# Kernel tuning notes

Measured on AMD Instinct MI355X. Metric: run time of the kernel, lower is better.

The kernel has to match this reference:

```python
import jax, jax.numpy as jnp
import numpy as np

B, S, D, MD = 4, 4096, 1024, 512
SCALE = 0.02  # init scale for weights


def _layernorm(x, g, b, eps=1e-5):
    m = jnp.mean(x, axis=-1, keepdims=True)
    v = jnp.mean((x - m) ** 2, axis=-1, keepdims=True)
    return (x - m) * jax.lax.rsqrt(v + eps) * g + b


def _mem_mlp(h, W0, W1):
    # MemoryMLP depth=2: linear -> gelu -> linear (no biases)
    return jax.nn.gelu(h @ W0) @ W1


def _assoc_scan(gates, inputs):
    # state_t = g_t * state_{t-1} + in_t, over the seq axis (axis=1)
    def step(state, gi):
        g, i = gi
        s = g * state + i
        return s, s
    init = jnp.zeros_like(inputs[:, 0])
    _, out = jax.lax.scan(step, init, (jnp.moveaxis(gates, 1, 0), jnp.moveaxis(inputs, 1, 0)))
    return jnp.moveaxis(out, 1, 0)


def setup_inputs() -> dict:
    key = jax.random.key(0)
    ks = jax.random.split(key, 10)
    return {
        "x": jax.random.normal(ks[0], (B, S, D), jnp.float32),
        "Wd": jax.random.normal(ks[1], (D, MD), jnp.float32) * SCALE,
        "bd": jnp.zeros((MD,), jnp.float32),
        "Wu": jax.random.normal(ks[2], (MD, D), jnp.float32) * SCALE,
        "bu": jnp.zeros((D,), jnp.float32),
        "Wq": jax.random.normal(ks[3], (MD, MD), jnp.float32) * SCALE,
        "bq": jnp.zeros((MD,), jnp.float32),
        "Wk": jax.random.normal(ks[4], (MD, MD), jnp.float32) * SCALE,
        "bk": jnp.zeros((MD,), jnp.float32),
        "Wv": jax.random.normal(ks[5], (MD, MD), jnp.float32) * SCALE,
        "bv": jnp.zeros((MD,), jnp.float32),
        "q_gamma": jnp.ones((MD,), jnp.float32),
        "q_beta": jnp.zeros((MD,), jnp.float32),
        "k_gamma": jnp.ones((MD,), jnp.float32),
        "k_beta": jnp.zeros((MD,), jnp.float32),
        "W0": jax.random.normal(ks[6], (MD, MD), jnp.float32) * SCALE,
        "W1": jax.random.normal(ks[7], (MD, MD), jnp.float32) * SCALE,
        "adaptive_lr": jnp.full((1,), 0.01, jnp.float32),
        "forget_factor": jnp.full((1,), 0.1, jnp.float32),
    }


def reference(x, Wd, bd, Wu, bu, Wq, bq, Wk, bk, Wv, bv,
              q_gamma, q_beta, k_gamma, k_beta, W0, W1,
              adaptive_lr, forget_factor):
    h = x @ Wd + bd                                   # [B,S,MD] down_proj
    q = _layernorm(h @ Wq + bq, q_gamma, q_beta)      # q_norm(to_queries)
    k = _layernorm(h @ Wk + bk, k_gamma, k_beta)      # k_norm(to_keys)
    v = h @ Wv + bv                                   # to_values
    retrieved = _mem_mlp(q, W0, W1)                   # memory read
    pred = _mem_mlp(k, W0, W1)                        # memory store pred
    # per-token surprise: MSE over feature dim
    surprise = jnp.mean((pred - v) ** 2, axis=-1, keepdims=True)  # [B,S,1]
    gate_val = 1.0 - jax.nn.sigmoid(forget_factor)[0]
    gates = jnp.full((B, S, 1), 1.0, jnp.float32) * gate_val
    inputs = adaptive_lr[0] * surprise * v            # surprise-weighted write
    scanned = _assoc_scan(gates, inputs)              # sequential recurrence
    out = (retrieved + scanned) @ Wu + bu             # up_proj
    return out
```

## Files before the change

### kernel.cpp

```cpp
#include <hip/hip_runtime.h>
#include <hip/hip_bf16.h>
#include <math.h>

#define B_    4
#define S_    4096
#define DD    1024
#define MD    512
#define NTOK  16384
#define CHUNK 32
#define NCH   128

typedef unsigned short u16;
typedef unsigned int u32;
typedef __attribute__((ext_vector_type(8))) short short8;
typedef __attribute__((ext_vector_type(4))) float f32x4;
typedef __attribute__((ext_vector_type(4))) unsigned short us4;

__device__ __forceinline__ float bf2f(u16 u) {
    u32 x = ((u32)u) << 16;
    return __builtin_bit_cast(float, x);
}
__device__ __forceinline__ u16 f2bf(float f) {
    u32 x = __builtin_bit_cast(u32, f);
    u32 lsb = (x >> 16) & 1u;
    x += 0x7fffu + lsb;
    return (u16)(x >> 16);
}
__device__ __forceinline__ float gelu_f(float x) {
    float x3 = x * x * x;
    return 0.5f * x * (1.0f + tanhf(0.7978845608028654f * (x + 0.044715f * x3)));
}
__device__ __forceinline__ float gate_from_ff(const float* ff) {
    return 1.0f - 1.0f / (1.0f + expf(-ff[0]));
}

#define GLDS(gp, lp) __builtin_amdgcn_global_load_lds( \
    (const __attribute__((address_space(1))) void*)(gp), \
    (__attribute__((address_space(3))) void*)(lp), 16, 0, 0)

template<int EPI, int HB, int OUTBF>
__global__ __launch_bounds__(256) void gemm_bf16_k(
    const u16* __restrict__ A0, const u16* __restrict__ A1, const u16* __restrict__ A2,
    const u16* __restrict__ W0p, const u16* __restrict__ W1p, const u16* __restrict__ W2p,
    const float* __restrict__ c0, const float* __restrict__ c1, const float* __restrict__ c2,
    void* __restrict__ o0, void* __restrict__ o1, void* __restrict__ o2,
    int K, int gx, int OM)
{
    __shared__ __align__(16) u16 Al[3][128 * 32];
    __shared__ __align__(16) u16 Bl[3][128 * 32];
    const int tid = threadIdx.x;
    const int w = tid >> 6, l = tid & 63;

    const int z = blockIdx.z;
    const u16* A      = (z == 0) ? A0 : (z == 1) ? A1 : A2;
    const u16* BT     = (z == 0) ? W0p : (z == 1) ? W1p : W2p;
    const float* bias = (z == 0) ? c0 : (z == 1) ? c1 : c2;
    void* outp        = (z == 0) ? o0 : (z == 1) ? o1 : o2;

    const int nwg = gridDim.x;
    const int cpx = nwg >> 3;
    const int o = blockIdx.x;
    const int swz = (o & 7) * cpx + (o >> 3);
    const int bx = swz % gx, by = swz / gx;

    const int rowBase = by * 128, colBase = bx * 128;
    const int wm = (w >> 1) * 64, wn = (w & 1) * 64;
    const int lr = l & 15;

    float bj[4] = {0.f, 0.f, 0.f, 0.f};
    if (HB) {
#pragma unroll
        for (int n = 0; n < 4; ++n) bj[n] = bias[colBase + wn + n * 16 + lr];
        asm volatile("" :: "v"(bj[0]), "v"(bj[1]), "v"(bj[2]), "v"(bj[3]));
    }
    asm volatile("s_waitcnt vmcnt(0)" ::: "memory");
    __builtin_amdgcn_sched_barrier(0);

    const int srow = l >> 2;
    const int skoff = ((l & 3) ^ (srow & 3)) * 8;
    const u16* Ag0 = A  + (size_t)(rowBase + w * 16 + srow) * K + skoff;
    const u16* Ag1 = A  + (size_t)(rowBase + (w + 4) * 16 + srow) * K + skoff;
    const u16* Bg0 = BT + (size_t)(colBase + w * 16 + srow) * K + skoff;
    const u16* Bg1 = BT + (size_t)(colBase + (w + 4) * 16 + srow) * K + skoff;

    f32x4 acc[4][4];
#pragma unroll
    for (int i = 0; i < 4; ++i)
#pragma unroll
        for (int j = 0; j < 4; ++j) acc[i][j] = (f32x4){0.f, 0.f, 0.f, 0.f};

    const int KT = K >> 5;

#define STAGE(kt, buf) do { \
    const size_t ko = (size_t)(kt) << 5; \
    GLDS(Ag0 + ko, &Al[buf][(w * 16) * 32]); \
    GLDS(Ag1 + ko, &Al[buf][((w + 4) * 16) * 32]); \
    GLDS(Bg0 + ko, &Bl[buf][(w * 16) * 32]); \
    GLDS(Bg1 + ko, &Bl[buf][((w + 4) * 16) * 32]); \
} while (0)

    STAGE(0, 0);
    STAGE(1, 1);
    asm volatile("s_waitcnt vmcnt(4)" ::: "memory");
    __builtin_amdgcn_sched_barrier(0);
    __builtin_amdgcn_s_barrier();
    __builtin_amdgcn_sched_barrier(0);

    const int rsw = (((l >> 4) ^ (l & 3)) << 3);
    int bt = 0;
    for (int t = 0; t < KT; ++t) {
        int bs = bt + 2; if (bs >= 3) bs -= 3;
        const bool more = (t + 2) < KT;
        if (more) STAGE(t + 2, bs);
        short8 af[4], bfr[4];
#pragma unroll
        for (int m = 0; m < 4; ++m)
            af[m] = *(const short8*)&Al[bt][(wm + m * 16 + lr) * 32 + rsw];
#pragma unroll
        for (int n = 0; n < 4; ++n)
            bfr[n] = *(const short8*)&Bl[bt][(wn + n * 16 + lr) * 32 + rsw];
#pragma unroll
        for (int m = 0; m < 4; ++m)
#pragma unroll
            for (int n = 0; n < 4; ++n)
                acc[m][n] = __builtin_amdgcn_mfma_f32_16x16x32_bf16(af[m], bfr[n], acc[m][n], 0, 0, 0);
        if (more) { asm volatile("s_waitcnt vmcnt(4)" ::: "memory"); }
        else      { asm volatile("s_waitcnt vmcnt(0)" ::: "memory"); }
        __builtin_amdgcn_sched_barrier(0);
        __builtin_amdgcn_s_barrier();
        __builtin_amdgcn_sched_barrier(0);
        bt = (bt + 1 == 3) ? 0 : bt + 1;
    }
#undef STAGE

    const int g4 = (l >> 4) * 4;
    const int col0 = colBase + wn;

    if (OUTBF) {
        u16* scr = &Al[0][0] + w * 1024;
        u16* ob = (u16*)outp;
        const bool odd = l & 1;
        const int lrp = lr & ~1;
#pragma unroll
        for (int m = 0; m < 4; ++m) {
            const int baseRow = rowBase + wm + m * 16;
            float vq[4][4];
#pragma unroll
            for (int n = 0; n < 4; ++n) {
#pragma unroll
                for (int q = 0; q < 4; ++q) {
                    float vv = acc[m][n][q] + bj[n];
                    if (EPI == 1) vv = gelu_f(vv);
                    vq[n][q] = vv;
                }
            }
#pragma unroll
            for (int n = 0; n < 4; ++n) {
                float pv[4];
#pragma unroll
                for (int q = 0; q < 4; ++q) pv[q] = __shfl_xor(vq[n][q], 1);
                const int q0 = odd ? 2 : 0;
#pragma unroll
                for (int j = 0; j < 2; ++j) {
                    const int qq = q0 + j;
                    float lo = odd ? pv[qq] : vq[n][qq];
                    float hi = odd ? vq[n][qq] : pv[qq];
                    u32 word = (u32)f2bf(lo) | ((u32)f2bf(hi) << 16);
                    *(u32*)&scr[(g4 + qq) * 64 + n * 16 + lrp] = word;
                }
            }
            asm volatile("s_waitcnt lgkmcnt(0)" ::: "memory");
            __builtin_amdgcn_sched_barrier(0);
            short8 r0 = *(const short8*)&scr[(l >> 3) * 64 + (l & 7) * 8];
            short8 r1 = *(const short8*)&scr[((l >> 3) + 8) * 64 + (l & 7) * 8];
            const size_t gaddr = (size_t)(baseRow + (l >> 3)) * OM + col0 + (l & 7) * 8;
            *(short8*)(ob + gaddr) = r0;
            *(short8*)(ob + gaddr + (size_t)8 * OM) = r1;
            __builtin_amdgcn_sched_barrier(0);
        }
    } else {
#pragma unroll
        for (int n = 0; n < 4; ++n) {
            const int col = col0 + n * 16 + lr;
#pragma unroll
            for (int m = 0; m < 4; ++m) {
                const int row0 = rowBase + wm + m * 16 + g4;
#pragma unroll
                for (int q = 0; q < 4; ++q) {
                    float vv = acc[m][n][q] + bj[n];
                    if (EPI == 1) vv = gelu_f(vv);
                    ((float*)outp)[(size_t)(row0 + q) * OM + col] = vv;
                }
            }
        }
    }
}

__global__ __launch_bounds__(256) void cvt_bf16_k(const float* __restrict__ in,
                                                  u16* __restrict__ out, int n)
{
    size_t i = ((size_t)blockIdx.x * 256 + threadIdx.x) * 8;
    if (i + 8 > (size_t)n) return;
    float4 a = *(const float4*)(in + i);
    float4 b = *(const float4*)(in + i + 4);
    short8 o;
    o[0] = (short)f2bf(a.x); o[1] = (short)f2bf(a.y);
    o[2] = (short)f2bf(a.z); o[3] = (short)f2bf(a.w);
    o[4] = (short)f2bf(b.x); o[5] = (short)f2bf(b.y);
    o[6] = (short)f2bf(b.z); o[7] = (short)f2bf(b.w);
    *(short8*)(out + i) = o;
}

__global__ __launch_bounds__(256) void wtrans_k(const float* __restrict__ W,
                                                u16* __restrict__ WT, int K, int M)
{
    __shared__ float t[32][33];
    const int tx = threadIdx.x, ty = threadIdx.y;
    const int m0 = blockIdx.x * 32, k0 = blockIdx.y * 32;
#pragma unroll
    for (int i = 0; i < 4; ++i)
        t[ty + i * 8][tx] = W[(size_t)(k0 + ty + i * 8) * M + m0 + tx];
    __syncthreads();
#pragma unroll
    for (int i = 0; i < 4; ++i)
        WT[(size_t)(m0 + ty + i * 8) * K + k0 + tx] = f2bf(t[tx][ty + i * 8]);
}

__global__ __launch_bounds__(256) void wtrans5_k(
    const float* __restrict__ Wa, const float* __restrict__ Wb,
    const float* __restrict__ Wc, const float* __restrict__ Wd_,
    const float* __restrict__ We,
    u16* __restrict__ Ta, u16* __restrict__ Tb, u16* __restrict__ Tc,
    u16* __restrict__ Td, u16* __restrict__ Te)
{
    __shared__ float t[32][33];
    const float* W; u16* T;
    switch (blockIdx.z) {
        case 0: W = Wa; T = Ta; break;
        case 1: W = Wb; T = Tb; break;
        case 2: W = Wc; T = Tc; break;
        case 3: W = Wd_; T = Td; break;
        default: W = We; T = Te; break;
    }
    const int tx = threadIdx.x, ty = threadIdx.y;
    const int m0 = blockIdx.x * 32, k0 = blockIdx.y * 32;
#pragma unroll
    for (int i = 0; i < 4; ++i)
        t[ty + i * 8][tx] = W[(size_t)(k0 + ty + i * 8) * 512 + m0 + tx];
    __syncthreads();
#pragma unroll
    for (int i = 0; i < 4; ++i)
        T[(size_t)(m0 + ty + i * 8) * 512 + k0 + tx] = f2bf(t[tx][ty + i * 8]);
}

__global__ __launch_bounds__(256) void ln2_k(u16* __restrict__ X0, u16* __restrict__ X1,
                                             const float* __restrict__ g0, const float* __restrict__ b0,
                                             const float* __restrict__ g1, const float* __restrict__ b1)
{
    const int row = blockIdx.x, tid = threadIdx.x;
    u16* x = (blockIdx.y ? X1 : X0) + (size_t)row * MD;
    const float* g = blockIdx.y ? g1 : g0;
    const float* b = blockIdx.y ? b1 : b0;
    float v0 = bf2f(x[tid]), v1 = bf2f(x[tid + 256]);
    float s = v0 + v1, q = v0 * v0 + v1 * v1;
#pragma unroll
    for (int off = 32; off > 0; off >>= 1) {
        s += __shfl_down(s, off);
        q += __shfl_down(q, off);
    }
    __shared__ float redS[4], redQ[4];
    __shared__ float s_mean, s_rstd;
    const int lane = tid & 63, w = tid >> 6;
    if (lane == 0) { redS[w] = s; redQ[w] = q; }
    __syncthreads();
    if (tid == 0) {
        float S = redS[0] + redS[1] + redS[2] + redS[3];
        float Q = redQ[0] + redQ[1] + redQ[2] + redQ[3];
        float m = S * (1.f / 512.f);
        float var = Q * (1.f / 512.f) - m * m;
        s_mean = m; s_rstd = rsqrtf(var + 1e-5f);
    }
    __syncthreads();
    const float m = s_mean, rs = s_rstd;
    x[tid]       = f2bf((v0 - m) * rs * g[tid]       + b[tid]);
    x[tid + 256] = f2bf((v1 - m) * rs * g[tid + 256] + b[tid + 256]);
}

__global__ __launch_bounds__(256) void surprise_k(const u16* __restrict__ pred,
                                                  const u16* __restrict__ v,
                                                  const float* __restrict__ lr_p,
                                                  float* __restrict__ coef)
{
    const int row = blockIdx.x, tid = threadIdx.x;
    const u16* pp = pred + (size_t)row * MD;
    const u16* vp = v + (size_t)row * MD;
    float d0 = bf2f(pp[tid]) - bf2f(vp[tid]);
    float d1 = bf2f(pp[tid + 256]) - bf2f(vp[tid + 256]);
    float q = d0 * d0 + d1 * d1;
#pragma unroll
    for (int off = 32; off > 0; off >>= 1) q += __shfl_down(q, off);
    __shared__ float redQ[4];
    const int lane = tid & 63, w = tid >> 6;
    if (lane == 0) redQ[w] = q;
    __syncthreads();
    if (tid == 0) {
        float Q = redQ[0] + redQ[1] + redQ[2] + redQ[3];
        coef[row] = lr_p[0] * (Q * (1.f / 512.f));
    }
}

__global__ __launch_bounds__(256) void scan1_k(u16* __restrict__ io,
                                               const float* __restrict__ coef,
                                               const float* __restrict__ ff,
                                               float* __restrict__ carry)
{
    const int idx = blockIdx.x * blockDim.x + threadIdx.x;
    const int d4 = (idx & 127) * 4;
    const int c = (idx >> 7) & (NCH - 1);
    const int b = idx >> 14;
    const float g = gate_from_ff(ff);
    const int tok0 = b * S_ + c * CHUNK;
    u16* p = io + (size_t)tok0 * MD + d4;
    const float* cf = coef + tok0;
    float s0 = 0.f, s1 = 0.f, s2 = 0.f, s3 = 0.f;
#pragma unroll 4
    for (int t = 0; t < CHUNK; ++t) {
        us4 vv = *(const us4*)(p + (size_t)t * MD);
        const float ct = cf[t];
        s0 = fmaf(g, s0, ct * bf2f(vv.x));
        s1 = fmaf(g, s1, ct * bf2f(vv.y));
        s2 = fmaf(g, s2, ct * bf2f(vv.z));
        s3 = fmaf(g, s3, ct * bf2f(vv.w));
        us4 ov = { f2bf(s0), f2bf(s1), f2bf(s2), f2bf(s3) };
        *(us4*)(p + (size_t)t * MD) = ov;
    }
    float4 cw = { s0, s1, s2, s3 };
    *(float4*)(carry + ((size_t)b * NCH + c) * MD + d4) = cw;
}

__global__ __launch_bounds__(256) void scan2_k(const float* __restrict__ carry,
                                               const float* __restrict__ ff,
                                               float* __restrict__ Sin)
{
    const int idx = blockIdx.x * blockDim.x + threadIdx.x;
    const int d = idx & (MD - 1);
    const int b = idx >> 9;
    const float g = gate_from_ff(ff);
    const float gL = powf(g, (float)CHUNK);
    float p = 0.f;
    for (int c = 0; c < NCH; ++c) {
        Sin[((size_t)b * NCH + c) * MD + d] = p;
        p = carry[((size_t)b * NCH + c) * MD + d] + gL * p;
    }
}

__global__ __launch_bounds__(256) void scan3_k(const u16* __restrict__ loc,
                                               const float* __restrict__ Sin,
                                               const u16* __restrict__ retr,
                                               const float* __restrict__ ff,
                                               u16* __restrict__ fin)
{
    const size_t idx = (size_t)blockIdx.x * blockDim.x + threadIdx.x;
    const int d4 = (int)(idx & 127) * 4;
    const int t = (int)((idx >> 7) & (S_ - 1));
    const int b = (int)(idx >> 19);
    const int c = t >> 5, tl = t & (CHUNK - 1);
    const float g = gate_from_ff(ff);
    const float f = exp2f((float)(tl + 1) * log2f(g));
    const size_t row = (size_t)(b * S_ + t) * MD + d4;
    us4 lv = *(const us4*)(loc + row);
    us4 rv = *(const us4*)(retr + row);
    float4 sv = *(const float4*)(Sin + ((size_t)b * NCH + c) * MD + d4);
    us4 ov;
    ov.x = f2bf(bf2f(lv.x) + f * sv.x + bf2f(rv.x));
    ov.y = f2bf(bf2f(lv.y) + f * sv.y + bf2f(rv.y));
    ov.z = f2bf(bf2f(lv.z) + f * sv.z + bf2f(rv.z));
    ov.w = f2bf(bf2f(lv.w) + f * sv.w + bf2f(rv.w));
    *(us4*)(fin + row) = ov;
}

extern "C" void kernel_launch(void* const* d_in, const int* in_sizes, int n_in,
                              void* d_out, int out_size, void* d_ws, size_t ws_size,
                              hipStream_t stream) {
    const float* x   = (const float*)d_in[0];
    const float* Wd  = (const float*)d_in[1];
    const float* bd  = (const float*)d_in[2];
    const float* Wu  = (const float*)d_in[3];
    const float* bu  = (const float*)d_in[4];
    const float* Wq  = (const float*)d_in[5];
    const float* bq  = (const float*)d_in[6];
    const float* Wk  = (const float*)d_in[7];
    const float* bk  = (const float*)d_in[8];
    const float* Wv  = (const float*)d_in[9];
    const float* bv  = (const float*)d_in[10];
    const float* qg  = (const float*)d_in[11];
    const float* qb  = (const float*)d_in[12];
    const float* kg  = (const float*)d_in[13];
    const float* kb  = (const float*)d_in[14];
    const float* W0  = (const float*)d_in[15];
    const float* W1  = (const float*)d_in[16];
    const float* lr  = (const float*)d_in[17];
    const float* ff  = (const float*)d_in[18];
    float* out = (float*)d_out;

    u16* wdT   = (u16*)d_ws;
    u16* wqT   = wdT + 512 * 1024;
    u16* wkT   = wqT + 512 * 512;
    u16* wvT   = wkT + 512 * 512;
    u16* w0T   = wvT + 512 * 512;
    u16* w1T   = w0T + 512 * 512;
    u16* wuT   = w1T + 512 * 512;
    u16* xb    = wuT + 1024 * 512;
    u16* hb    = xb + (size_t)NTOK * DD;
    u16* b1    = hb + (size_t)NTOK * MD;
    u16* b2    = b1 + (size_t)NTOK * MD;
    u16* VB    = b2 + (size_t)NTOK * MD;
    float* coef  = (float*)(VB + (size_t)NTOK * MD);
    float* carry = coef + NTOK;
    float* Sin   = carry + (size_t)B_ * NCH * MD;
    u16* ax0 = xb;
    u16* ax1 = xb + (size_t)NTOK * MD;

    dim3 blk(256);
    dim3 t32(32, 8);

    cvt_bf16_k<<<(NTOK * DD) / (256 * 8), blk, 0, stream>>>(x, xb, NTOK * DD);
    wtrans_k<<<dim3(16, 32), t32, 0, stream>>>(Wd, wdT, 1024, 512);
    wtrans5_k<<<dim3(16, 16, 5), t32, 0, stream>>>(Wq, Wk, Wv, W0, W1,
        wqT, wkT, wvT, w0T, w1T);
    wtrans_k<<<dim3(32, 16), t32, 0, stream>>>(Wu, wuT, 512, 1024);

    gemm_bf16_k<0, 1, 1><<<dim3(512, 1, 1), blk, 0, stream>>>(
        xb, xb, xb, wdT, wdT, wdT, bd, bd, bd, hb, hb, hb, 1024, 4, 512);
    gemm_bf16_k<0, 1, 1><<<dim3(512, 1, 3), blk, 0, stream>>>(
        hb, hb, hb, wqT, wkT, wvT, bq, bk, bv, b1, b2, VB, 512, 4, 512);
    ln2_k<<<dim3(NTOK, 2), blk, 0, stream>>>(b1, b2, qg, qb, kg, kb);
    gemm_bf16_k<1, 0, 1><<<dim3(512, 1, 2), blk, 0, stream>>>(
        b1, b2, b2, w0T, w0T, w0T, nullptr, nullptr, nullptr, ax0, ax1, ax1, 512, 4, 512);
    gemm_bf16_k<0, 0, 1><<<dim3(512, 1, 2), blk, 0, stream>>>(
        ax0, ax1, ax1, w1T, w1T, w1T, nullptr, nullptr, nullptr, b1, b2, b2, 512, 4, 512);
    surprise_k<<<NTOK, blk, 0, stream>>>(b2, VB, lr, coef);
    scan1_k<<<(B_ * NCH * (MD / 4)) / 256, blk, 0, stream>>>(VB, coef, ff, carry);
    scan2_k<<<(B_ * MD) / 256, blk, 0, stream>>>(carry, ff, Sin);
    scan3_k<<<(NTOK * (MD / 4)) / 256, blk, 0, stream>>>(VB, Sin, b1, ff, hb);
    gemm_bf16_k<0, 1, 0><<<dim3(1024, 1, 1), blk, 0, stream>>>(
        hb, hb, hb, wuT, wuT, wuT, bu, bu, bu, out, out, out, 512, 8, 1024);
}
```

Baseline: 329.6 us.

## Use 256x128 GEMM tiles with 8 warps and drop grid swizzle

Doubles the GEMM block to 512 threads and the M tile to 256 rows. Each warp now stages two A slices and one B slice, and the wait counts are adjusted to match. The L2-friendly block-index swizzle is replaced by a plain 2D grid. This halves the number of blocks and raises B-tile reuse per block, at the cost of more LDS per block, fewer blocks for load balance, and losing the swizzled access order.

```diff
diff --git a/kernel.cpp b/kernel.cpp
--- a/kernel.cpp
+++ b/kernel.cpp
@@ -39,14 +39,14 @@
     (__attribute__((address_space(3))) void*)(lp), 16, 0, 0)
 
 template<int EPI, int HB, int OUTBF>
-__global__ __launch_bounds__(256) void gemm_bf16_k(
+__global__ __launch_bounds__(512) void gemm_bf16_k(
     const u16* __restrict__ A0, const u16* __restrict__ A1, const u16* __restrict__ A2,
     const u16* __restrict__ W0p, const u16* __restrict__ W1p, const u16* __restrict__ W2p,
     const float* __restrict__ c0, const float* __restrict__ c1, const float* __restrict__ c2,
     void* __restrict__ o0, void* __restrict__ o1, void* __restrict__ o2,
-    int K, int gx, int OM)
-{
-    __shared__ __align__(16) u16 Al[3][128 * 32];
+    int K, int OM)
+{
+    __shared__ __align__(16) u16 Al[3][256 * 32];
     __shared__ __align__(16) u16 Bl[3][128 * 32];
     const int tid = threadIdx.x;
     const int w = tid >> 6, l = tid & 63;
@@ -57,13 +57,7 @@
     const float* bias = (z == 0) ? c0 : (z == 1) ? c1 : c2;
     void* outp        = (z == 0) ? o0 : (z == 1) ? o1 : o2;
 
-    const int nwg = gridDim.x;
-    const int cpx = nwg >> 3;
-    const int o = blockIdx.x;
-    const int swz = (o & 7) * cpx + (o >> 3);
-    const int bx = swz % gx, by = swz / gx;
-
-    const int rowBase = by * 128, colBase = bx * 128;
+    const int rowBase = blockIdx.y * 256, colBase = blockIdx.x * 128;
     const int wm = (w >> 1) * 64, wn = (w & 1) * 64;
     const int lr = l & 15;
 
@@ -78,10 +72,9 @@
 
     const int srow = l >> 2;
     const int skoff = ((l & 3) ^ (srow & 3)) * 8;
-    const u16* Ag0 = A  + (size_t)(rowBase + w * 16 + srow) * K + skoff;
-    const u16* Ag1 = A  + (size_t)(rowBase + (w + 4) * 16 + srow) * K + skoff;
+    const u16* Ag0 = A  + (size_t)(rowBase + (2 * w) * 16 + srow) * K + skoff;
+    const u16* Ag1 = A  + (size_t)(rowBase + (2 * w + 1) * 16 + srow) * K + skoff;
     const u16* Bg0 = BT + (size_t)(colBase + w * 16 + srow) * K + skoff;
-    const u16* Bg1 = BT + (size_t)(colBase + (w + 4) * 16 + srow) * K + skoff;
 
     f32x4 acc[4][4];
 #pragma unroll
@@ -93,15 +86,14 @@
 
 #define STAGE(kt, buf) do { \
     const size_t ko = (size_t)(kt) << 5; \
-    GLDS(Ag0 + ko, &Al[buf][(w * 16) * 32]); \
-    GLDS(Ag1 + ko, &Al[buf][((w + 4) * 16) * 32]); \
+    GLDS(Ag0 + ko, &Al[buf][((2 * w) * 16) * 32]); \
+    GLDS(Ag1 + ko, &Al[buf][((2 * w + 1) * 16) * 32]); \
     GLDS(Bg0 + ko, &Bl[buf][(w * 16) * 32]); \
-    GLDS(Bg1 + ko, &Bl[buf][((w + 4) * 16) * 32]); \
 } while (0)
 
     STAGE(0, 0);
     STAGE(1, 1);
-    asm volatile("s_waitcnt vmcnt(4)" ::: "memory");
+    asm volatile("s_waitcnt vmcnt(3)" ::: "memory");
     __builtin_amdgcn_sched_barrier(0);
     __builtin_amdgcn_s_barrier();
     __builtin_amdgcn_sched_barrier(0);
@@ -124,7 +116,7 @@
 #pragma unroll
             for (int n = 0; n < 4; ++n)
                 acc[m][n] = __builtin_amdgcn_mfma_f32_16x16x32_bf16(af[m], bfr[n], acc[m][n], 0, 0, 0);
-        if (more) { asm volatile("s_waitcnt vmcnt(4)" ::: "memory"); }
+        if (more) { asm volatile("s_waitcnt vmcnt(3)" ::: "memory"); }
         else      { asm volatile("s_waitcnt vmcnt(0)" ::: "memory"); }
         __builtin_amdgcn_sched_barrier(0);
         __builtin_amdgcn_s_barrier();
@@ -422,6 +414,7 @@
     u16* ax1 = xb + (size_t)NTOK * MD;
 
     dim3 blk(256);
+    dim3 gblk(512);
     dim3 t32(32, 8);
 
     cvt_bf16_k<<<(NTOK * DD) / (256 * 8), blk, 0, stream>>>(x, xb, NTOK * DD);
@@ -430,19 +423,19 @@
         wqT, wkT, wvT, w0T, w1T);
     wtrans_k<<<dim3(32, 16), t32, 0, stream>>>(Wu, wuT, 512, 1024);
 
-    gemm_bf16_k<0, 1, 1><<<dim3(512, 1, 1), blk, 0, stream>>>(
-        xb, xb, xb, wdT, wdT, wdT, bd, bd, bd, hb, hb, hb, 1024, 4, 512);
-    gemm_bf16_k<0, 1, 1><<<dim3(512, 1, 3), blk, 0, stream>>>(
-        hb, hb, hb, wqT, wkT, wvT, bq, bk, bv, b1, b2, VB, 512, 4, 512);
+    gemm_bf16_k<0, 1, 1><<<dim3(4, 64, 1), gblk, 0, stream>>>(
+        xb, xb, xb, wdT, wdT, wdT, bd, bd, bd, hb, hb, hb, 1024, 512);
+    gemm_bf16_k<0, 1, 1><<<dim3(4, 64, 3), gblk, 0, stream>>>(
+        hb, hb, hb, wqT, wkT, wvT, bq, bk, bv, b1, b2, VB, 512, 512);
     ln2_k<<<dim3(NTOK, 2), blk, 0, stream>>>(b1, b2, qg, qb, kg, kb);
-    gemm_bf16_k<1, 0, 1><<<dim3(512, 1, 2), blk, 0, stream>>>(
-        b1, b2, b2, w0T, w0T, w0T, nullptr, nullptr, nullptr, ax0, ax1, ax1, 512, 4, 512);
-    gemm_bf16_k<0, 0, 1><<<dim3(512, 1, 2), blk, 0, stream>>>(
-        ax0, ax1, ax1, w1T, w1T, w1T, nullptr, nullptr, nullptr, b1, b2, b2, 512, 4, 512);
+    gemm_bf16_k<1, 0, 1><<<dim3(4, 64, 2), gblk, 0, stream>>>(
+        b1, b2, b2, w0T, w0T, w0T, nullptr, nullptr, nullptr, ax0, ax1, ax1, 512, 512);
+    gemm_bf16_k<0, 0, 1><<<dim3(4, 64, 2), gblk, 0, stream>>>(
+        ax0, ax1, ax1, w1T, w1T, w1T, nullptr, nullptr, nullptr, b1, b2, b2, 512, 512);
     surprise_k<<<NTOK, blk, 0, stream>>>(b2, VB, lr, coef);
     scan1_k<<<(B_ * NCH * (MD / 4)) / 256, blk, 0, stream>>>(VB, coef, ff, carry);
     scan2_k<<<(B_ * MD) / 256, blk, 0, stream>>>(carry, ff, Sin);
     scan3_k<<<(NTOK * (MD / 4)) / 256, blk, 0, stream>>>(VB, Sin, b1, ff, hb);
-    gemm_bf16_k<0, 1, 0><<<dim3(1024, 1, 1), blk, 0, stream>>>(
-        hb, hb, hb, wuT, wuT, wuT, bu, bu, bu, out, out, out, 512, 8, 1024);
-}
+    gemm_bf16_k<0, 1, 0><<<dim3(8, 64, 1), gblk, 0, stream>>>(
+        hb, hb, hb, wuT, wuT, wuT, bu, bu, bu, out, out, out, 512, 1024);
+}
```

Measured after the change: 341.4 us. +3.6%, slower.
